# Kernel optimization log

Measured on AMD Instinct MI355X. Metric: run time of the kernel, lower is better.

Reference implementation:

```python
import jax, jax.numpy as jnp
import numpy as np

B, N, E, H = 8, 2048, 1024, 16
D = E // H

def setup_inputs() -> dict:
    key = jax.random.key(0)
    kx, kw1, kb1, kw2, kb2 = jax.random.split(key, 5)
    scale = 0.02
    return {
        "x": jax.random.normal(kx, (B, N, E), dtype=jnp.float32),
        "Wqkv": jax.random.normal(kw1, (3 * E, E), dtype=jnp.float32) * scale,
        "bqkv": jax.random.normal(kb1, (3 * E,), dtype=jnp.float32) * scale,
        "Wo": jax.random.normal(kw2, (E, E), dtype=jnp.float32) * scale,
        "bo": jax.random.normal(kb2, (E,), dtype=jnp.float32) * scale,
    }

def reference(x, Wqkv, bqkv, Wo, bo):
    b, n, e = x.shape
    h, d = H, D
    # qkv projection: torch Linear is x @ W.T + b
    qkv = x @ Wqkv.T + bqkv                                   # [B,N,3E]
    qkv = qkv.reshape(b, n, 3, h, d).transpose(2, 0, 3, 1, 4)  # [3,B,H,N,D]
    q, k, v = qkv[0], qkv[1], qkv[2]                           # each [B,H,N,D]
    # NOTE: replicates the original's einsum labeling exactly: with q,k of
    # shape [B,H,N,D], 'nqhd,nkhd->nhqk' contracts over D and yields [B,N,H,H]
    # (softmax over the head axis), matching the torch source bit-for-bit.
    energy = jnp.einsum('nqhd,nkhd->nhqk', q, k)               # [B,N,H,H]
    attention = jax.nn.softmax(energy / jnp.sqrt(jnp.float32(e)), axis=-1)
    out = jnp.einsum('nhql,nlhd->nqhd', attention, v)          # [B,H,N,D]
    out = out.reshape(b, n, e)                                 # same raw-buffer reshape as torch
    return out @ Wo.T + bo
```

## Files before the change

### kernel.cpp

```cpp
#include <hip/hip_runtime.h>
#include <hip/hip_bf16.h>
#include <stdint.h>


typedef __attribute__((ext_vector_type(8))) short short8;
typedef __attribute__((ext_vector_type(8))) unsigned short ushort8;
typedef __attribute__((ext_vector_type(16))) float floatx16;

__device__ __forceinline__ unsigned short f2bf(float f) {
  union { float f; uint32_t u; } x; x.f = f;
  uint32_t u = x.u;
  return (unsigned short)((u + 0x7fffu + ((u >> 16) & 1u)) >> 16);
}
__device__ __forceinline__ float bf2f(unsigned short s) {
  union { uint32_t u; float f; } x; x.u = ((uint32_t)s) << 16; return x.f;
}
__device__ __forceinline__ void unpack8(uint4 u, float* f) {
  f[0] = bf2f((unsigned short)(u.x & 0xffffu)); f[1] = bf2f((unsigned short)(u.x >> 16));
  f[2] = bf2f((unsigned short)(u.y & 0xffffu)); f[3] = bf2f((unsigned short)(u.y >> 16));
  f[4] = bf2f((unsigned short)(u.z & 0xffffu)); f[5] = bf2f((unsigned short)(u.z >> 16));
  f[6] = bf2f((unsigned short)(u.w & 0xffffu)); f[7] = bf2f((unsigned short)(u.w >> 16));
}

__global__ __launch_bounds__(256) void cvt_all(const float* __restrict__ x,
                                               const float* __restrict__ w1,
                                               const float* __restrict__ w2,
                                               unsigned short* __restrict__ xb,
                                               unsigned short* __restrict__ w1b,
                                               unsigned short* __restrict__ w2b) {
  int i = blockIdx.x * 256 + threadIdx.x;
  const float* src;
  unsigned short* dst;
  if (i < 2097152) {
    src = x; dst = xb;
  } else if (i < 2097152 + 393216) {
    i -= 2097152; src = w1; dst = w1b;
  } else {
    i -= 2490368; src = w2; dst = w2b;
  }
  long base = (long)i * 8;
  const float4* p = (const float4*)(src + base);
  float4 a = p[0], b = p[1];
  ushort8 r;
  r[0] = f2bf(a.x); r[1] = f2bf(a.y); r[2] = f2bf(a.z); r[3] = f2bf(a.w);
  r[4] = f2bf(b.x); r[5] = f2bf(b.y); r[6] = f2bf(b.z); r[7] = f2bf(b.w);
  *(ushort8*)(dst + base) = r;
}

__device__ __forceinline__ void gl2lds16(const void* g, void* l) {
  __builtin_amdgcn_global_load_lds(
      (const uint32_t __attribute__((address_space(1)))*)g,
      (uint32_t __attribute__((address_space(3)))*)(uint32_t)(uintptr_t)l,
      16, 0, 0);
}

template <bool OUT_BF16>
__device__ __forceinline__ void gemm_core(const unsigned short* __restrict__ A,
                                          const unsigned short* __restrict__ Bm,
                                          const float* __restrict__ bias,
                                          void* __restrict__ Cout, int N, int K) {
  __shared__ __align__(16) unsigned short lA[128 * 64];
  __shared__ __align__(16) unsigned short lB[128 * 64];
  const int tid = threadIdx.x;
  const int lane = tid & 63;
  const int wave = tid >> 6;
  const long row0 = (long)blockIdx.y * 128;
  const long col0 = (long)blockIdx.x * 128;
  const int wr = (wave & 1) * 64;
  const int wc = (wave >> 1) * 64;
  const int l32 = lane & 31;
  const int lhi = lane >> 5;
  const int l7 = lane & 7;

  floatx16 acc[2][2] = {};

  const int rstage = tid >> 3;
  const int cstage = (tid & 7) ^ (rstage & 7);
  const unsigned short* gA0 = A + (row0 + rstage) * (long)K + cstage * 8;
  const unsigned short* gB0 = Bm + (col0 + rstage) * (long)K + cstage * 8;
  char* ldsA0 = (char*)lA + tid * 16;
  char* ldsB0 = (char*)lB + tid * 16;
  const long rowstep = (long)32 * K;

  int aRow[2], bRow[2], sOff[4];
#pragma unroll
  for (int i = 0; i < 2; i++) aRow[i] = (wr + i * 32 + l32) * 128;
#pragma unroll
  for (int j = 0; j < 2; j++) bRow[j] = (wc + j * 32 + l32) * 128;
#pragma unroll
  for (int s = 0; s < 4; s++) sOff[s] = ((2 * s + lhi) ^ l7) * 16;

  for (int k0 = 0; k0 < K; k0 += 64) {
    __syncthreads();
#pragma unroll
    for (int p = 0; p < 4; p++) {
      gl2lds16(gA0 + p * rowstep + k0, ldsA0 + p * 4096);
      gl2lds16(gB0 + p * rowstep + k0, ldsB0 + p * 4096);
    }
    __syncthreads();

#pragma unroll
    for (int s = 0; s < 4; s++) {
      short8 a0 = *(const short8*)((char*)lA + aRow[0] + sOff[s]);
      short8 a1 = *(const short8*)((char*)lA + aRow[1] + sOff[s]);
      short8 b0 = *(const short8*)((char*)lB + bRow[0] + sOff[s]);
      short8 b1 = *(const short8*)((char*)lB + bRow[1] + sOff[s]);
      acc[0][0] = __builtin_amdgcn_mfma_f32_32x32x16_bf16(a0, b0, acc[0][0], 0, 0, 0);
      acc[0][1] = __builtin_amdgcn_mfma_f32_32x32x16_bf16(a0, b1, acc[0][1], 0, 0, 0);
      acc[1][0] = __builtin_amdgcn_mfma_f32_32x32x16_bf16(a1, b0, acc[1][0], 0, 0, 0);
      acc[1][1] = __builtin_amdgcn_mfma_f32_32x32x16_bf16(a1, b1, acc[1][1], 0, 0, 0);
    }
  }

  float bv[2];
#pragma unroll
  for (int j = 0; j < 2; j++) bv[j] = bias[col0 + wc + j * 32 + l32];

#pragma unroll
  for (int i = 0; i < 2; i++) {
#pragma unroll
    for (int j = 0; j < 2; j++) {
      const long col = col0 + wc + j * 32 + l32;
      const long rbase = row0 + wr + i * 32 + 4 * lhi;
#pragma unroll
      for (int reg = 0; reg < 16; reg++) {
        const long row = rbase + (reg & 3) + 8 * (reg >> 2);
        float v = acc[i][j][reg] + bv[j];
        if (OUT_BF16)
          ((unsigned short*)Cout)[row * N + col] = f2bf(v);
        else
          ((float*)Cout)[row * N + col] = v;
      }
    }
  }
}

__global__ __launch_bounds__(256) void gemm_qkv(const unsigned short* __restrict__ A,
                                                const unsigned short* __restrict__ Bm,
                                                const float* __restrict__ bias,
                                                unsigned short* __restrict__ Cout,
                                                int N, int K) {
  gemm_core<true>(A, Bm, bias, Cout, N, K);
}

__global__ __launch_bounds__(256) void gemm_out(const unsigned short* __restrict__ A,
                                                const unsigned short* __restrict__ Bm,
                                                const float* __restrict__ bias,
                                                float* __restrict__ Cout,
                                                int N, int K) {
  gemm_core<false>(A, Bm, bias, Cout, N, K);
}

__global__ __launch_bounds__(256) void attn_kernel(const unsigned short* __restrict__ qkv,
                                                   unsigned short* __restrict__ out2) {
  const int t = blockIdx.x * 256 + threadIdx.x;
  const int sub = t & 3;
  const int pair = t >> 2;
  const int head = pair & 15;
  const int token = pair >> 4;
  const int b = token >> 11;
  const int s = token & 2047;
  const unsigned short* base = qkv + (long)token * 3072;

  float qf[16];
  {
    const uint4* qp = (const uint4*)(base + head * 64 + sub * 16);
    unpack8(qp[0], qf);
    unpack8(qp[1], qf + 8);
  }

  float e[16];
  const unsigned short* kbase = base + 1024 + sub * 16;
  for (int j = 0; j < 16; j++) {
    const uint4* kp = (const uint4*)(kbase + j * 64);
    float kf[16];
    unpack8(kp[0], kf);
    unpack8(kp[1], kf + 8);
    float a0 = 0.f, a1 = 0.f, a2 = 0.f, a3 = 0.f;
#pragma unroll
    for (int c = 0; c < 4; c++) {
      a0 += qf[c] * kf[c];
      a1 += qf[c + 4] * kf[c + 4];
      a2 += qf[c + 8] * kf[c + 8];
      a3 += qf[c + 12] * kf[c + 12];
    }
    float ej = (a0 + a1) + (a2 + a3);
    ej += __shfl_xor(ej, 1);
    ej += __shfl_xor(ej, 2);
    e[j] = ej * 0.03125f;
  }

  float mx = e[0];
#pragma unroll
  for (int j = 1; j < 16; j++) mx = fmaxf(mx, e[j]);
  float sum = 0.f;
#pragma unroll
  for (int j = 0; j < 16; j++) { e[j] = __expf(e[j] - mx); sum += e[j]; }
  const float inv = 1.f / sum;

  float o[16];
#pragma unroll
  for (int d = 0; d < 16; d++) o[d] = 0.f;
  const unsigned short* vbase = base + 2048 + sub * 16;
  for (int j = 0; j < 16; j++) {
    const float wgt = e[j] * inv;
    const uint4* vp = (const uint4*)(vbase + j * 64);
    float vf[16];
    unpack8(vp[0], vf);
    unpack8(vp[1], vf + 8);
#pragma unroll
    for (int d = 0; d < 16; d++) o[d] += wgt * vf[d];
  }

  const long row = (long)b * 2048 + head * 128 + (s >> 4);
  unsigned short* op = out2 + row * 1024 + (long)(s & 15) * 64 + sub * 16;
#pragma unroll
  for (int w = 0; w < 2; w++) {
    ushort8 r;
#pragma unroll
    for (int c = 0; c < 8; c++) r[c] = f2bf(o[w * 8 + c]);
    *(ushort8*)(op + w * 8) = r;
  }
}

extern "C" void kernel_launch(void* const* d_in, const int* in_sizes, int n_in,
                              void* d_out, int out_size, void* d_ws, size_t ws_size,
                              hipStream_t stream) {
  const float* x    = (const float*)d_in[0];
  const float* Wqkv = (const float*)d_in[1];
  const float* bqkv = (const float*)d_in[2];
  const float* Wo   = (const float*)d_in[3];
  const float* bo   = (const float*)d_in[4];
  float* out = (float*)d_out;

  char* ws = (char*)d_ws;
  unsigned short* x_bf    = (unsigned short*)(ws);
  unsigned short* wqkv_bf = (unsigned short*)(ws + 33554432);
  unsigned short* wo_bf   = (unsigned short*)(ws + 39845888);
  unsigned short* qkv_bf  = (unsigned short*)(ws + 41943040);
  unsigned short* out2_bf = (unsigned short*)(ws + 142606336);

  cvt_all<<<10240, 256, 0, stream>>>(x, Wqkv, Wo, x_bf, wqkv_bf, wo_bf);

  dim3 g1(3072 / 128, 16384 / 128);
  gemm_qkv<<<g1, 256, 0, stream>>>(x_bf, wqkv_bf, bqkv, qkv_bf, 3072, 1024);

  attn_kernel<<<4096, 256, 0, stream>>>(qkv_bf, out2_bf);

  dim3 g2(1024 / 128, 16384 / 128);
  gemm_out<<<g2, 256, 0, stream>>>(out2_bf, wo_bf, bo, out, 1024, 1024);
}
```

Before: 340.9 us.

## Split QKV GEMM into three launches and stage attention token rows in LDS

The fused QKV projection GEMM is split into three separate launches (Q, K, V), each writing its slice of the qkv buffer through a column offset and leading dimension. The attention kernel now maps one wave per token and copies the whole 6 KB qkv row into LDS with global_load_lds before computing. This replaces scattered global reads of the shared K/V rows with coalesced copies. The split adds launch overhead and gives smaller grids per launch. The attention kernel gains an LDS round trip and a block-wide barrier.

Measured after the change: 408.1 us. +19.7%, slower.

```diff
diff --git a/kernel.cpp b/kernel.cpp
--- a/kernel.cpp
+++ b/kernel.cpp
@@ -58,7 +58,8 @@
 __device__ __forceinline__ void gemm_core(const unsigned short* __restrict__ A,
                                           const unsigned short* __restrict__ Bm,
                                           const float* __restrict__ bias,
-                                          void* __restrict__ Cout, int N, int K) {
+                                          void* __restrict__ Cout, int K,
+                                          int colOff, int ldc) {
   __shared__ __align__(16) unsigned short lA[128 * 64];
   __shared__ __align__(16) unsigned short lB[128 * 64];
   const int tid = threadIdx.x;
@@ -120,59 +121,76 @@
   for (int i = 0; i < 2; i++) {
 #pragma unroll
     for (int j = 0; j < 2; j++) {
-      const long col = col0 + wc + j * 32 + l32;
+      const long col = colOff + col0 + wc + j * 32 + l32;
       const long rbase = row0 + wr + i * 32 + 4 * lhi;
 #pragma unroll
       for (int reg = 0; reg < 16; reg++) {
         const long row = rbase + (reg & 3) + 8 * (reg >> 2);
         float v = acc[i][j][reg] + bv[j];
         if (OUT_BF16)
-          ((unsigned short*)Cout)[row * N + col] = f2bf(v);
+          ((unsigned short*)Cout)[row * ldc + col] = f2bf(v);
         else
-          ((float*)Cout)[row * N + col] = v;
+          ((float*)Cout)[row * ldc + col] = v;
       }
     }
   }
 }
 
-__global__ __launch_bounds__(256) void gemm_qkv(const unsigned short* __restrict__ A,
-                                                const unsigned short* __restrict__ Bm,
-                                                const float* __restrict__ bias,
-                                                unsigned short* __restrict__ Cout,
-                                                int N, int K) {
-  gemm_core<true>(A, Bm, bias, Cout, N, K);
-}
-
+__global__ __launch_bounds__(256) void gemm_q(const unsigned short* __restrict__ A,
+                                              const unsigned short* __restrict__ Bm,
+                                              const float* __restrict__ bias,
+                                              unsigned short* __restrict__ Cout, int K) {
+  gemm_core<true>(A, Bm, bias, Cout, K, 0, 3072);
+}
+__global__ __launch_bounds__(256) void gemm_k(const unsigned short* __restrict__ A,
+                                              const unsigned short* __restrict__ Bm,
+                                              const float* __restrict__ bias,
+                                              unsigned short* __restrict__ Cout, int K) {
+  gemm_core<true>(A, Bm, bias, Cout, K, 1024, 3072);
+}
+__global__ __launch_bounds__(256) void gemm_v(const unsigned short* __restrict__ A,
+                                              const unsigned short* __restrict__ Bm,
+                                              const float* __restrict__ bias,
+                                              unsigned short* __restrict__ Cout, int K) {
+  gemm_core<true>(A, Bm, bias, Cout, K, 2048, 3072);
+}
 __global__ __launch_bounds__(256) void gemm_out(const unsigned short* __restrict__ A,
                                                 const unsigned short* __restrict__ Bm,
                                                 const float* __restrict__ bias,
-                                                float* __restrict__ Cout,
-                                                int N, int K) {
-  gemm_core<false>(A, Bm, bias, Cout, N, K);
+                                                float* __restrict__ Cout, int K) {
+  gemm_core<false>(A, Bm, bias, Cout, K, 0, 1024);
 }
 
 __global__ __launch_bounds__(256) void attn_kernel(const unsigned short* __restrict__ qkv,
                                                    unsigned short* __restrict__ out2) {
-  const int t = blockIdx.x * 256 + threadIdx.x;
-  const int sub = t & 3;
-  const int pair = t >> 2;
-  const int head = pair & 15;
-  const int token = pair >> 4;
+  __shared__ __align__(16) char lds[4 * 6144];
+  const int tid = threadIdx.x;
+  const int wave = tid >> 6;
+  const int lane = tid & 63;
+  const int token = blockIdx.x * 4 + wave;
+  const int head = lane >> 2;
+  const int sub = lane & 3;
   const int b = token >> 11;
   const int s = token & 2047;
-  const unsigned short* base = qkv + (long)token * 3072;
+
+  const char* gbase = (const char*)qkv + (long)token * 6144;
+  char* lbase = lds + wave * 6144;
+#pragma unroll
+  for (int p = 0; p < 6; p++)
+    gl2lds16(gbase + p * 1024 + lane * 16, lbase + p * 1024 + lane * 16);
+  __syncthreads();
 
   float qf[16];
   {
-    const uint4* qp = (const uint4*)(base + head * 64 + sub * 16);
+    const uint4* qp = (const uint4*)(lbase + head * 128 + sub * 32);
     unpack8(qp[0], qf);
     unpack8(qp[1], qf + 8);
   }
 
   float e[16];
-  const unsigned short* kbase = base + 1024 + sub * 16;
+  const char* kbase = lbase + 2048 + sub * 32;
   for (int j = 0; j < 16; j++) {
-    const uint4* kp = (const uint4*)(kbase + j * 64);
+    const uint4* kp = (const uint4*)(kbase + j * 128);
     float kf[16];
     unpack8(kp[0], kf);
     unpack8(kp[1], kf + 8);
@@ -201,10 +219,10 @@
   float o[16];
 #pragma unroll
   for (int d = 0; d < 16; d++) o[d] = 0.f;
-  const unsigned short* vbase = base + 2048 + sub * 16;
+  const char* vbase = lbase + 4096 + sub * 32;
   for (int j = 0; j < 16; j++) {
     const float wgt = e[j] * inv;
-    const uint4* vp = (const uint4*)(vbase + j * 64);
+    const uint4* vp = (const uint4*)(vbase + j * 128);
     float vf[16];
     unpack8(vp[0], vf);
     unpack8(vp[1], vf + 8);
@@ -242,11 +260,13 @@
 
   cvt_all<<<10240, 256, 0, stream>>>(x, Wqkv, Wo, x_bf, wqkv_bf, wo_bf);
 
-  dim3 g1(3072 / 128, 16384 / 128);
-  gemm_qkv<<<g1, 256, 0, stream>>>(x_bf, wqkv_bf, bqkv, qkv_bf, 3072, 1024);
+  dim3 gp(1024 / 128, 16384 / 128);
+  gemm_q<<<gp, 256, 0, stream>>>(x_bf, wqkv_bf,               bqkv,        qkv_bf, 1024);
+  gemm_k<<<gp, 256, 0, stream>>>(x_bf, wqkv_bf + 1024 * 1024, bqkv + 1024, qkv_bf, 1024);
+  gemm_v<<<gp, 256, 0, stream>>>(x_bf, wqkv_bf + 2048 * 1024, bqkv + 2048, qkv_bf, 1024);
 
   attn_kernel<<<4096, 256, 0, stream>>>(qkv_bf, out2_bf);
 
   dim3 g2(1024 / 128, 16384 / 128);
-  gemm_out<<<g2, 256, 0, stream>>>(out2_bf, wo_bf, bo, out, 1024, 1024);
-}
+  gemm_out<<<g2, 256, 0, stream>>>(out2_bf, wo_bf, bo, out, 1024);
+}
```
